# Optimization experiments

Hardware: AMD Instinct MI355X
Metric: run time of the kernel (lower is better)

The kernel has to match this reference:

```python
import jax, jax.numpy as jnp
import numpy as np

INP = 512
HIDDEN = 512
N_HEADS = 8          # called 'head_dim' in the torch code
D_HEAD = HIDDEN // N_HEADS  # 64
BASE = 10000.0
SCALE = D_HEAD ** (-0.5)


def rope(x):
    # x: [b, s, h, d]
    b, s, h, d = x.shape
    half = d // 2
    theta = 1.0 / (BASE ** (jnp.arange(0, d, 2, dtype=jnp.float32) / d))  # [d/2]
    idx_theta = jnp.arange(s, dtype=jnp.float32)[:, None] * theta[None, :]  # [s, d/2]
    idx_theta2 = jnp.concatenate([idx_theta, idx_theta], axis=1)            # [s, d]
    neg_half = jnp.concatenate([-x[..., half:], x[..., :half]], axis=-1)
    cos = jnp.cos(idx_theta2)[None, :, None, :]
    sin = jnp.sin(idx_theta2)[None, :, None, :]
    return x * cos + neg_half * sin


def setup_inputs() -> dict:
    key = jax.random.key(0)
    ks = jax.random.split(key, 10)
    b, s = 4, 2048
    init = lambda k, shp, fan_in: jax.random.normal(k, shp, jnp.float32) * (fan_in ** -0.5)
    return {
        "x": jax.random.normal(ks[0], (b, s, INP), jnp.float32),
        "c": jax.random.normal(ks[1], (b, s, INP), jnp.float32),
        "Wq": init(ks[2], (INP, HIDDEN), INP), "bq": jnp.zeros((HIDDEN,), jnp.float32),
        "Wk": init(ks[3], (INP, HIDDEN), INP), "bk": jnp.zeros((HIDDEN,), jnp.float32),
        "Wv": init(ks[4], (INP, HIDDEN), INP), "bv": jnp.zeros((HIDDEN,), jnp.float32),
        "Wo": init(ks[5], (HIDDEN, INP), HIDDEN), "bo": jnp.zeros((INP,), jnp.float32),
    }


def reference(x, c, Wq, bq, Wk, bk, Wv, bv, Wo, bo):
    b, s, _ = x.shape
    h_res = x
    q = (c @ Wq + bq).reshape(b, s, N_HEADS, D_HEAD)
    k = (x @ Wk + bk).reshape(b, s, N_HEADS, D_HEAD)
    v = (x @ Wv + bv).reshape(b, s, N_HEADS, D_HEAD)
    q = rope(q)
    k = rope(k)  # computed but unused, exactly as in the source
    # NOTE: source computes scores between q and V (not k) -- faithful reproduction
    att = jnp.einsum('bihd,bjhd->bhij', q, v)            # [b, h, s, s]
    att = jax.nn.softmax(att * SCALE, axis=-1)
    out = jnp.einsum('bhij,bjhd->bihd', att, v)          # [b, s, h, d]
    out = out.reshape(b, s, HIDDEN)
    out = out @ Wo + bo
    return out + h_res
```

## Files before the change

### kernel.cpp

```cpp
#include <hip/hip_runtime.h>
#include <hip/hip_bf16.h>
#include <cstdint>

typedef float f32x4 __attribute__((ext_vector_type(4)));
typedef float f32x16 __attribute__((ext_vector_type(16)));
typedef short bf16x8 __attribute__((ext_vector_type(8)));
typedef short bf16x4 __attribute__((ext_vector_type(4)));
typedef unsigned int u32x2 __attribute__((ext_vector_type(2)));
typedef unsigned short u16;

#define B_    4
#define S_    2048
#define H_    8
#define D_    64
#define M_    8192

#define OFF_CBF   0UL
#define OFF_XBF   8388608UL
#define OFF_QBH   16777216UL
#define OFF_VBH   25165824UL
#define OFF_VTBH  33554432UL
#define OFF_ATTN  41943040UL
#define OFF_WQT   50331648UL
#define OFF_WVT   50855936UL
#define OFF_WOT   51380224UL
#define OFF_BIAS  51904512UL
#define OFF_COS   51910656UL
#define OFF_SIN   52172800UL
#define WS_NEEDED 52434944UL

__device__ __forceinline__ u16 f2bf(float f){
    union { float f; uint32_t u; } v; v.f = f;
    uint32_t r = (v.u + 0x7fffu + ((v.u >> 16) & 1u)) >> 16;
    return (u16)r;
}
__device__ __forceinline__ float bf2f(u16 h){
    union { uint32_t u; float f; } v; v.u = ((uint32_t)h) << 16;
    return v.f;
}

__device__ __forceinline__ uint32_t cvtpk(float lo, float hi){
    uint32_t r;
    asm("v_cvt_pk_bf16_f32 %0, %1, %2" : "=v"(r) : "v"(lo), "v"(hi));
    return r;
}
__device__ __forceinline__ void plswap(uint32_t &va, uint32_t &vb){
#if __has_builtin(__builtin_amdgcn_permlane32_swap)
    u32x2 r = __builtin_amdgcn_permlane32_swap(va, vb, false, false);
    va = r[0]; vb = r[1];
#else
    asm volatile("v_permlane32_swap_b32 %0, %1" : "+v"(va), "+v"(vb));
#endif
}

__device__ __forceinline__ int swz(int row, int col){
    return (col & ~63) | ((((col >> 3) & 7) ^ (row & 7)) << 3) | (col & 7);
}

__device__ __forceinline__ int detect_f32(const void* x_in){
    int lane = threadIdx.x & 63;
    ushort2 dv = ((const ushort2*)x_in)[lane];
    bool hit = ((((dv.x >> 7) & 0xFF) >= 160) || (((dv.y >> 7) & 0xFF) >= 160));
    return __ballot(hit) != 0ULL;
}

__device__ __forceinline__ void gload_lds16(const u16* g, u16* l){
    __builtin_amdgcn_global_load_lds(
        (const __attribute__((address_space(1))) void*)g,
        (__attribute__((address_space(3))) void*)l, 16, 0, 0);
}

__global__ void k_prep(const void* c_in, const void* x_in,
                       const void* Wq, const void* Wv, const void* Wo,
                       const void* bq, const void* bv, const void* bo,
                       u16* c_bf, u16* x_bf,
                       u16* Wqt, u16* Wvt, u16* Wot, float* bias_ws,
                       float* cos_t, float* sin_t){
    int bid = blockIdx.x;
    if (bid >= 11264){
        int idx = (bid - 11264) * 256 + threadIdx.x;
        int pos = idx >> 5, j = idx & 31;
        double theta = pow(10000.0, -(double)j / 32.0);
        double rev = ((double)pos * theta) * 0.15915494309189535;
        rev -= floor(rev);
        float fr = (float)rev;
        cos_t[idx] = __builtin_amdgcn_cosf(fr);
        sin_t[idx] = __builtin_amdgcn_sinf(fr);
        return;
    }
    if (bid >= 8192){
        int f = detect_f32(x_in);
        int wi = (bid - 8192) >> 10;
        int idx = ((bid - 8192) & 1023) * 256 + threadIdx.x;
        int k = idx >> 9, n = idx & 511;
        const void* W; u16* Wt; const void* bb;
        if (wi == 0){ W = Wq; Wt = Wqt; bb = bq; }
        else if (wi == 1){ W = Wv; Wt = Wvt; bb = bv; }
        else { W = Wo; Wt = Wot; bb = bo; }
        float v = f ? ((const float*)W)[idx] : bf2f(((const u16*)W)[idx]);
        Wt[n * 512 + (wi == 2 ? k : swz(n, k))] = f2bf(v);
        if (idx < 512){
            float b = f ? ((const float*)bb)[idx] : bf2f(((const u16*)bb)[idx]);
            bias_ws[wi * 512 + idx] = b;
        }
        return;
    }
    int f = detect_f32(x_in);
    int isx = bid >= 4096;
    int t = (bid & 4095) * 256 + threadIdx.x;
    const void* src = isx ? x_in : c_in;
    u16* dst = isx ? x_bf : c_bf;
    int e0 = t * 4, row = e0 >> 9, col = e0 & 511;
    size_t didx = (size_t)row * 512 + swz(row, col);
    ushort4 o;
    if (f){
        float4 v = ((const float4*)src)[t];
        o.x = f2bf(v.x); o.y = f2bf(v.y); o.z = f2bf(v.z); o.w = f2bf(v.w);
    } else {
        o = ((const ushort4*)src)[t];
    }
    *(ushort4*)(dst + didx) = o;
}

__global__ __launch_bounds__(256) void k_gemm_qv(
    const u16* __restrict__ c_bf, const u16* __restrict__ x_bf,
    const u16* __restrict__ Wqt, const u16* __restrict__ Wvt,
    const float* __restrict__ bias_ws,
    const float* __restrict__ cos_t, const float* __restrict__ sin_t,
    u16* __restrict__ Qbh, u16* __restrict__ Vbh, u16* __restrict__ Vtbh)
{
    __shared__ __align__(16) u16 Als[2][128 * 64];
    __shared__ __align__(16) u16 Bls[2][128 * 64];
    const int w = threadIdx.x >> 6, lane = threadIdx.x & 63;
    const int g = lane >> 4, cq = lane & 15;
    const int wm = w & 1, wn = w >> 1;
    const int z = blockIdx.z;
    const u16* A  = z ? x_bf : c_bf;
    const u16* Wt = z ? Wvt : Wqt;
    const float* bias = bias_ws + (z ? 512 : 0);
    const int m0b = blockIdx.x * 128, n0b = blockIdx.y * 128;
    const int m0 = m0b + wm * 64, n0 = n0b + wn * 64;
    const int swzi = ((cq & 7) << 3);

    int srow[4], scol[4];
    #pragma unroll
    for (int i = 0; i < 4; i++){
        int flat = (w * 4 + i) * 64 + lane;
        srow[i] = flat >> 3; scol[i] = (flat & 7) * 8;
    }

    const f32x4 zero = {0.f, 0.f, 0.f, 0.f};
    f32x4 acc[4][4];
    #pragma unroll
    for (int i = 0; i < 4; i++)
        #pragma unroll
        for (int j = 0; j < 4; j++) acc[i][j] = zero;

    #pragma unroll
    for (int i = 0; i < 4; i++){
        gload_lds16(A  + (size_t)(m0b + srow[i]) * 512 + scol[i], &Als[0][(w*4 + i) * 512]);
        gload_lds16(Wt + (size_t)(n0b + srow[i]) * 512 + scol[i], &Bls[0][(w*4 + i) * 512]);
    }

    for (int kt = 0; kt < 8; kt++){
        const int buf = kt & 1;
        __builtin_amdgcn_s_waitcnt(0x0F70);
        __syncthreads();
        if (kt < 7){
            const int kk = (kt + 1) * 64;
            #pragma unroll
            for (int i = 0; i < 4; i++){
                gload_lds16(A  + (size_t)(m0b + srow[i]) * 512 + kk + scol[i], &Als[buf^1][(w*4 + i) * 512]);
                gload_lds16(Wt + (size_t)(n0b + srow[i]) * 512 + kk + scol[i], &Bls[buf^1][(w*4 + i) * 512]);
            }
        }
        #pragma unroll
        for (int ks = 0; ks < 2; ks++){
            const int cs = ((ks * 4 + g) << 3) ^ swzi;
            bf16x8 a[4], b[4];
            #pragma unroll
            for (int mt = 0; mt < 4; mt++)
                a[mt] = *(const bf16x8*)&Als[buf][(wm*64 + mt*16 + cq) * 64 + cs];
            #pragma unroll
            for (int nt = 0; nt < 4; nt++)
                b[nt] = *(const bf16x8*)&Bls[buf][(wn*64 + nt*16 + cq) * 64 + cs];
            #pragma unroll
            for (int mt = 0; mt < 4; mt++)
                #pragma unroll
                for (int nt = 0; nt < 4; nt++)
                    acc[mt][nt] = __builtin_amdgcn_mfma_f32_16x16x32_bf16(a[mt], b[nt], acc[mt][nt], 0, 0, 0);
        }
    }
    __syncthreads();

    #pragma unroll
    for (int nt = 0; nt < 4; nt++){
        float bvv = bias[n0 + nt*16 + cq];
        #pragma unroll
        for (int mt = 0; mt < 4; mt++) acc[mt][nt] += bvv;
    }
    const int h = n0 >> 6;
    if (z == 0){
        const float SCL = 0.125f * 1.4426950408889634f;
        #pragma unroll
        for (int mt = 0; mt < 4; mt++){
            #pragma unroll
            for (int r = 0; r < 4; r++){
                int row = m0 + mt*16 + g*4 + r;
                int b_idx = row >> 11, si = row & 2047;
                size_t base = ((size_t)(b_idx*8 + h) * 2048 + si) * 64;
                #pragma unroll
                for (int nt = 0; nt < 2; nt++){
                    int dj = nt*16 + cq;
                    float cv = cos_t[si*32 + dj], sv = sin_t[si*32 + dj];
                    float x1 = acc[mt][nt][r], x2 = acc[mt][nt+2][r];
                    Qbh[base + dj]      = f2bf((x1*cv - x2*sv) * SCL);
                    Qbh[base + dj + 32] = f2bf((x2*cv + x1*sv) * SCL);
                }
            }
        }
    } else {
        float* ltw = ((float*)&Als[0][0]) + w * (16 * 65);
        const int b_idx = m0 >> 11, si0 = m0 & 2047;
        const size_t tbase = ((size_t)(b_idx*8 + h) * 64) * 2048;
        #pragma unroll
        for (int mt = 0; mt < 4; mt++)
            #pragma unroll
            for (int r = 0; r < 4; r++){
                int row = m0 + mt*16 + g*4 + r;
                int bi = row >> 11, si = row & 2047;
                size_t base = ((size_t)(bi*8 + h) * 2048 + si) * 64;
                #pragma unroll
                for (int nt = 0; nt < 4; nt++)
                    Vbh[base + nt*16 + cq] = f2bf(acc[mt][nt][r]);
            }
        #pragma unroll
        for (int nt = 0; nt < 4; nt++){
            #pragma unroll
            for (int mt = 0; mt < 4; mt++)
                #pragma unroll
                for (int r = 0; r < 4; r++)
                    ltw[cq * 65 + mt*16 + g*4 + r] = acc[mt][nt][r];
            __builtin_amdgcn_wave_barrier();
            #pragma unroll
            for (int dd = 0; dd < 16; dd++){
                float v = ltw[dd * 65 + lane];
                Vtbh[tbase + (size_t)(nt*16 + dd) * 2048 + si0 + lane] = f2bf(v);
            }
            __builtin_amdgcn_wave_barrier();
        }
    }
}

__global__ __launch_bounds__(256, 2) void k_attn(
    const u16* __restrict__ Qbh, const u16* __restrict__ Vbh,
    const u16* __restrict__ Vtbh,
    u16* __restrict__ part0, u16* __restrict__ part1, float* __restrict__ lsum)
{
    __shared__ __align__(16) u16 Vs[2][64 * 68];
    __shared__ __align__(16) u16 Vts[2][64 * 68];

    const int bid = blockIdx.x;
    const int logical = (bid & 7) * 64 + (bid >> 3);
    const int xb = logical & 7;
    const int bh = (logical >> 3) & 31;
    const int z  = logical >> 8;

    const int w = threadIdx.x >> 6, lane = threadIdx.x & 63;
    const int r32 = lane & 31, hl = lane >> 5;
    const int i0 = xb * 256 + w * 64;
    const int j0 = z * 1024;

    bf16x8 aq[2][4];
    #pragma unroll
    for (int it = 0; it < 2; it++)
        #pragma unroll
        for (int kk = 0; kk < 4; kk++)
            aq[it][kk] = *(const bf16x8*)(Qbh + ((size_t)bh*2048 + i0 + it*32 + r32)*64 + kk*16 + hl*8);

    const int sr = w * 16 + (lane >> 2), sc = (lane & 3) * 16;
    const u16* gvs = Vbh  + ((size_t)bh*2048 + j0 + sr) * 64 + sc;
    const u16* gvt = Vtbh + ((size_t)bh*64 + sr) * 2048 + j0 + sc;
    const int ls = sr * 68 + sc;

    {
        bf16x8 a0 = *(const bf16x8*)gvs,       a1 = *(const bf16x8*)(gvs + 8);
        bf16x8 b0 = *(const bf16x8*)gvt,       b1 = *(const bf16x8*)(gvt + 8);
        *(bf16x8*)&Vs[0][ls]  = a0;  *(bf16x8*)&Vs[0][ls + 8]  = a1;
        *(bf16x8*)&Vts[0][ls] = b0;  *(bf16x8*)&Vts[0][ls + 8] = b1;
    }

    f32x16 ot[2][2];
    #pragma unroll
    for (int it = 0; it < 2; it++)
        #pragma unroll
        for (int dt = 0; dt < 2; dt++)
            #pragma unroll
            for (int rr = 0; rr < 16; rr++) ot[it][dt][rr] = 0.f;
    const f32x16 zero16 = ot[0][0];
    float fl[2] = {0.f, 0.f};

    for (int jt = 0; jt < 16; jt++){
        const int buf = jt & 1;
        __syncthreads();
        bf16x8 na0, na1, nb0, nb1;
        if (jt < 15){
            na0 = *(const bf16x8*)(gvs + (size_t)(jt + 1) * 4096);
            na1 = *(const bf16x8*)(gvs + (size_t)(jt + 1) * 4096 + 8);
            nb0 = *(const bf16x8*)(gvt + (size_t)(jt + 1) * 64);
            nb1 = *(const bf16x8*)(gvt + (size_t)(jt + 1) * 64 + 8);
        }
        bf16x8 pb[2][4];
        #pragma unroll
        for (int jtile = 0; jtile < 2; jtile++){
            bf16x8 vf[4];
            #pragma unroll
            for (int kk = 0; kk < 4; kk++)
                vf[kk] = *(const bf16x8*)&Vs[buf][(jtile*32 + r32)*68 + kk*16 + hl*8];
            f32x16 st0 = zero16, st1 = zero16;
            __builtin_amdgcn_s_setprio(1);
            #pragma unroll
            for (int kk = 0; kk < 4; kk++){
                st0 = __builtin_amdgcn_mfma_f32_32x32x16_bf16(vf[kk], aq[0][kk], st0, 0, 0, 0);
                st1 = __builtin_amdgcn_mfma_f32_32x32x16_bf16(vf[kk], aq[1][kk], st1, 0, 0, 0);
            }
            __builtin_amdgcn_s_setprio(0);
            #pragma unroll
            for (int rr = 0; rr < 16; rr++) st0[rr] = __builtin_amdgcn_exp2f(st0[rr]);
            #pragma unroll
            for (int rr = 0; rr < 16; rr++) st1[rr] = __builtin_amdgcn_exp2f(st1[rr]);
            {
                float a0 = (st0[0]+st0[1]) + (st0[2]+st0[3]);
                float a1 = (st0[4]+st0[5]) + (st0[6]+st0[7]);
                float a2 = (st0[8]+st0[9]) + (st0[10]+st0[11]);
                float a3 = (st0[12]+st0[13]) + (st0[14]+st0[15]);
                fl[0] += (a0+a1) + (a2+a3);
                float b0 = (st1[0]+st1[1]) + (st1[2]+st1[3]);
                float b1 = (st1[4]+st1[5]) + (st1[6]+st1[7]);
                float b2 = (st1[8]+st1[9]) + (st1[10]+st1[11]);
                float b3 = (st1[12]+st1[13]) + (st1[14]+st1[15]);
                fl[1] += (b0+b1) + (b2+b3);
            }
            #pragma unroll
            for (int c = 0; c < 2; c++){
                uint32_t dA1 = cvtpk(st0[c*8+0], st0[c*8+1]);
                uint32_t dA2 = cvtpk(st0[c*8+2], st0[c*8+3]);
                uint32_t dB1 = cvtpk(st0[c*8+4], st0[c*8+5]);
                uint32_t dB2 = cvtpk(st0[c*8+6], st0[c*8+7]);
                plswap(dA1, dB1);
                plswap(dA2, dB2);
                union { bf16x8 v; uint32_t d[4]; } u;
                u.d[0] = dA1; u.d[1] = dA2; u.d[2] = dB1; u.d[3] = dB2;
                pb[0][jtile*2 + c] = u.v;
            }
            #pragma unroll
            for (int c = 0; c < 2; c++){
                uint32_t dA1 = cvtpk(st1[c*8+0], st1[c*8+1]);
                uint32_t dA2 = cvtpk(st1[c*8+2], st1[c*8+3]);
                uint32_t dB1 = cvtpk(st1[c*8+4], st1[c*8+5]);
                uint32_t dB2 = cvtpk(st1[c*8+6], st1[c*8+7]);
                plswap(dA1, dB1);
                plswap(dA2, dB2);
                union { bf16x8 v; uint32_t d[4]; } u;
                u.d[0] = dA1; u.d[1] = dA2; u.d[2] = dB1; u.d[3] = dB2;
                pb[1][jtile*2 + c] = u.v;
            }
        }
        __builtin_amdgcn_s_setprio(1);
        #pragma unroll
        for (int c = 0; c < 4; c++){
            bf16x8 vt0 = *(const bf16x8*)&Vts[buf][r32*68 + c*16 + hl*8];
            bf16x8 vt1 = *(const bf16x8*)&Vts[buf][(32 + r32)*68 + c*16 + hl*8];
            ot[0][0] = __builtin_amdgcn_mfma_f32_32x32x16_bf16(vt0, pb[0][c], ot[0][0], 0, 0, 0);
            ot[1][0] = __builtin_amdgcn_mfma_f32_32x32x16_bf16(vt0, pb[1][c], ot[1][0], 0, 0, 0);
            ot[0][1] = __builtin_amdgcn_mfma_f32_32x32x16_bf16(vt1, pb[0][c], ot[0][1], 0, 0, 0);
            ot[1][1] = __builtin_amdgcn_mfma_f32_32x32x16_bf16(vt1, pb[1][c], ot[1][1], 0, 0, 0);
        }
        __builtin_amdgcn_s_setprio(0);
        if (jt < 15){
            *(bf16x8*)&Vs[buf^1][ls]  = na0;  *(bf16x8*)&Vs[buf^1][ls + 8]  = na1;
            *(bf16x8*)&Vts[buf^1][ls] = nb0;  *(bf16x8*)&Vts[buf^1][ls + 8] = nb1;
        }
    }
    const int b_idx = bh >> 3, hh = bh & 7;
    u16* part = z ? part1 : part0;
    #pragma unroll
    for (int it = 0; it < 2; it++){
        float sum = fl[it] + __shfl_xor(fl[it], 32);
        const int row = b_idx*2048 + i0 + it*32 + r32;
        if (lane < 32)
            lsum[(size_t)z*65536 + (size_t)hh*8192 + row] = sum;
        #pragma unroll
        for (int dt = 0; dt < 2; dt++){
            #pragma unroll
            for (int q = 0; q < 4; q++){
                float v0 = ot[it][dt][q*4+0];
                float v1 = ot[it][dt][q*4+1];
                float v2 = ot[it][dt][q*4+2];
                float v3 = ot[it][dt][q*4+3];
                uint2 pw;
                pw.x = cvtpk(v0, v1);
                pw.y = cvtpk(v2, v3);
                int col = hh*64 + dt*32 + q*8 + hl*4;
                *(uint2*)&part[(size_t)row * 512 + col] = pw;
            }
        }
    }
}

__global__ __launch_bounds__(256) void k_gemm_out(
    const u16* __restrict__ part0, const u16* __restrict__ part1,
    const float* __restrict__ lsum,
    const u16* __restrict__ Wot, const float* __restrict__ bias_ws,
    const void* __restrict__ x_in, void* __restrict__ out)
{
    __shared__ __align__(16) u16 Als[2][128 * 68];
    __shared__ __align__(16) u16 Bls[2][64 * 68];
    const int w = threadIdx.x >> 6, lane = threadIdx.x & 63;
    const int g = lane >> 4, cq = lane & 15;
    const int wm = w & 1, wn = w >> 1;
    const int m0b = blockIdx.x * 128, n0b = blockIdx.y * 64;
    const int m0 = m0b + wm * 64, n0 = n0b + wn * 32;
    const int f = detect_f32(x_in);

    int sra[4], sca[4], srb[2], scb[2];
    #pragma unroll
    for (int i = 0; i < 4; i++){
        int flat = (w * 4 + i) * 64 + lane;
        sra[i] = flat >> 3; sca[i] = (flat & 7) * 8;
    }
    #pragma unroll
    for (int i = 0; i < 2; i++){
        int flat = (w * 2 + i) * 64 + lane;
        srb[i] = flat >> 3; scb[i] = (flat & 7) * 8;
    }

    const f32x4 zero = {0.f, 0.f, 0.f, 0.f};
    f32x4 acc[4][2];
    #pragma unroll
    for (int i = 0; i < 4; i++)
        #pragma unroll
        for (int j = 0; j < 2; j++) acc[i][j] = zero;

    bf16x8 pa0[4], pa1[4], pb[2]; float pr[4];
    #pragma unroll
    for (int i = 0; i < 4; i++){
        int row = m0b + sra[i];
        pa0[i] = *(const bf16x8*)&part0[(size_t)row * 512 + sca[i]];
        pa1[i] = *(const bf16x8*)&part1[(size_t)row * 512 + sca[i]];
        pr[i] = 1.f / (lsum[row] + lsum[65536 + row]);
    }
    #pragma unroll
    for (int i = 0; i < 2; i++)
        pb[i] = *(const bf16x8*)&Wot[(size_t)(n0b + srb[i]) * 512 + scb[i]];
    #pragma unroll
    for (int i = 0; i < 4; i++){
        union { bf16x8 v; u16 e[8]; } a8;
        #pragma unroll
        for (int e = 0; e < 8; e++)
            a8.e[e] = f2bf((bf2f((u16)pa0[i][e]) + bf2f((u16)pa1[i][e])) * pr[i]);
        *(bf16x8*)&Als[0][sra[i]*68 + sca[i]] = a8.v;
    }
    #pragma unroll
    for (int i = 0; i < 2; i++)
        *(bf16x8*)&Bls[0][srb[i]*68 + scb[i]] = pb[i];

    for (int kt = 0; kt < 8; kt++){
        const int buf = kt & 1;
        __syncthreads();
        if (kt < 7){
            const int kk = (kt + 1) * 64, h = kt + 1;
            #pragma unroll
            for (int i = 0; i < 4; i++){
                int row = m0b + sra[i];
                pa0[i] = *(const bf16x8*)&part0[(size_t)row * 512 + kk + sca[i]];
                pa1[i] = *(const bf16x8*)&part1[(size_t)row * 512 + kk + sca[i]];
                pr[i] = 1.f / (lsum[(size_t)h*8192 + row] + lsum[65536 + (size_t)h*8192 + row]);
            }
            #pragma unroll
            for (int i = 0; i < 2; i++)
                pb[i] = *(const bf16x8*)&Wot[(size_t)(n0b + srb[i]) * 512 + kk + scb[i]];
        }
        #pragma unroll
        for (int ks = 0; ks < 2; ks++){
            bf16x8 a[4], b[2];
            #pragma unroll
            for (int mt = 0; mt < 4; mt++)
                a[mt] = *(const bf16x8*)&Als[buf][(wm*64 + mt*16 + cq)*68 + ks*32 + g*8];
            #pragma unroll
            for (int nt = 0; nt < 2; nt++)
                b[nt] = *(const bf16x8*)&Bls[buf][(wn*32 + nt*16 + cq)*68 + ks*32 + g*8];
            #pragma unroll
            for (int mt = 0; mt < 4; mt++)
                #pragma unroll
                for (int nt = 0; nt < 2; nt++)
                    acc[mt][nt] = __builtin_amdgcn_mfma_f32_16x16x32_bf16(a[mt], b[nt], acc[mt][nt], 0, 0, 0);
        }
        if (kt < 7){
            #pragma unroll
            for (int i = 0; i < 4; i++){
                union { bf16x8 v; u16 e[8]; } a8;
                #pragma unroll
                for (int e = 0; e < 8; e++)
                    a8.e[e] = f2bf((bf2f((u16)pa0[i][e]) + bf2f((u16)pa1[i][e])) * pr[i]);
                *(bf16x8*)&Als[buf^1][sra[i]*68 + sca[i]] = a8.v;
            }
            #pragma unroll
            for (int i = 0; i < 2; i++)
                *(bf16x8*)&Bls[buf^1][srb[i]*68 + scb[i]] = pb[i];
        }
    }
    #pragma unroll
    for (int mt = 0; mt < 4; mt++)
        #pragma unroll
        for (int nt = 0; nt < 2; nt++)
            #pragma unroll
            for (int r = 0; r < 4; r++){
                int row = m0 + mt*16 + g*4 + r;
                int col = n0 + nt*16 + cq;
                size_t idx = (size_t)row * 512 + col;
                float resid = f ? ((const float*)x_in)[idx] : bf2f(((const u16*)x_in)[idx]);
                float v = acc[mt][nt][r] + bias_ws[1024 + col] + resid;
                if (f) ((float*)out)[idx] = v;
                else   ((u16*)out)[idx] = f2bf(v);
            }
}

extern "C" void kernel_launch(void* const* d_in, const int* in_sizes, int n_in,
                              void* d_out, int out_size, void* d_ws, size_t ws_size,
                              hipStream_t stream){
    const void* x_in = d_in[0];
    const void* c_in = d_in[1];
    const void* Wq = d_in[2]; const void* bq = d_in[3];
    const void* Wv = d_in[6]; const void* bv = d_in[7];
    const void* Wo = d_in[8]; const void* bo = d_in[9];

    if (ws_size < WS_NEEDED){
        hipMemsetAsync(d_out, 0, (size_t)out_size * 2, stream);
        return;
    }
    char* ws = (char*)d_ws;
    u16* c_bf  = (u16*)(ws + OFF_CBF);
    u16* x_bf  = (u16*)(ws + OFF_XBF);
    u16* Qbh   = (u16*)(ws + OFF_QBH);
    u16* Vbh   = (u16*)(ws + OFF_VBH);
    u16* Vtbh  = (u16*)(ws + OFF_VTBH);
    u16* part0 = (u16*)(ws + OFF_ATTN);
    u16* part1 = (u16*)(ws + OFF_CBF);
    float* lsum = (float*)(ws + OFF_XBF);
    u16* Wqt   = (u16*)(ws + OFF_WQT);
    u16* Wvt   = (u16*)(ws + OFF_WVT);
    u16* Wot   = (u16*)(ws + OFF_WOT);
    float* bias_ws = (float*)(ws + OFF_BIAS);
    float* cos_t   = (float*)(ws + OFF_COS);
    float* sin_t   = (float*)(ws + OFF_SIN);

    k_prep<<<11520, 256, 0, stream>>>(c_in, x_in, Wq, Wv, Wo, bq, bv, bo,
                                      c_bf, x_bf, Wqt, Wvt, Wot, bias_ws, cos_t, sin_t);
    k_gemm_qv<<<dim3(64, 4, 2), 256, 0, stream>>>(c_bf, x_bf, Wqt, Wvt, bias_ws,
                                                  cos_t, sin_t, Qbh, Vbh, Vtbh);
    k_attn<<<dim3(512), 256, 0, stream>>>(Qbh, Vbh, Vtbh, part0, part1, lsum);
    k_gemm_out<<<dim3(64, 8), 256, 0, stream>>>(part0, part1, lsum, Wot, bias_ws,
                                                x_in, d_out);
}
```

Before: 182.0 us.

## Software-pipeline attention loop so PV MFMAs of previous tile overlap next QV and exp

Restructures the attention main loop into a prologue, steady state, and epilogue. Each iteration now runs the P·V MFMAs for the previous tile, using the previous buffer, interleaved with the score MFMAs for the current tile, so matrix work overlaps the exp2 and packing work. The Q projection epilogue also stores Q in an interleaved packed layout with one cvt_pk per pair, and the attention kernel de-interleaves it on load. In exchange it adds an extra __syncthreads per iteration and raises register pressure because pb is live across iterations.

```diff
diff --git a/kernel.cpp b/kernel.cpp
--- a/kernel.cpp
+++ b/kernel.cpp
@@ -51,6 +51,24 @@
 #else
     asm volatile("v_permlane32_swap_b32 %0, %1" : "+v"(va), "+v"(vb));
 #endif
+}
+
+__device__ __forceinline__ f32x16 mfma32(bf16x8 a, bf16x8 b, f32x16 c){
+    return __builtin_amdgcn_mfma_f32_32x32x16_bf16(a, b, c, 0, 0, 0);
+}
+
+__device__ __forceinline__ void deint(uint4 a, uint4 b, bf16x8 &lo, bf16x8 &hi){
+    union { bf16x8 v; uint32_t d[4]; } L, H;
+    uint32_t s0=a.x, s1=a.y, s2=a.z, s3=a.w, s4=b.x, s5=b.y, s6=b.z, s7=b.w;
+    L.d[0] = (s0 & 0xffffu) | (s1 << 16);
+    L.d[1] = (s2 & 0xffffu) | (s3 << 16);
+    L.d[2] = (s4 & 0xffffu) | (s5 << 16);
+    L.d[3] = (s6 & 0xffffu) | (s7 << 16);
+    H.d[0] = (s0 >> 16) | (s1 & 0xffff0000u);
+    H.d[1] = (s2 >> 16) | (s3 & 0xffff0000u);
+    H.d[2] = (s4 >> 16) | (s5 & 0xffff0000u);
+    H.d[3] = (s6 >> 16) | (s7 & 0xffff0000u);
+    lo = L.v; hi = H.v;
 }
 
 __device__ __forceinline__ int swz(int row, int col){
@@ -202,20 +220,20 @@
     const int h = n0 >> 6;
     if (z == 0){
         const float SCL = 0.125f * 1.4426950408889634f;
+        uint32_t* Qpk = (uint32_t*)Qbh;
         #pragma unroll
         for (int mt = 0; mt < 4; mt++){
             #pragma unroll
             for (int r = 0; r < 4; r++){
                 int row = m0 + mt*16 + g*4 + r;
                 int b_idx = row >> 11, si = row & 2047;
-                size_t base = ((size_t)(b_idx*8 + h) * 2048 + si) * 64;
+                size_t base = ((size_t)(b_idx*8 + h) * 2048 + si) * 32;
                 #pragma unroll
                 for (int nt = 0; nt < 2; nt++){
                     int dj = nt*16 + cq;
                     float cv = cos_t[si*32 + dj], sv = sin_t[si*32 + dj];
                     float x1 = acc[mt][nt][r], x2 = acc[mt][nt+2][r];
-                    Qbh[base + dj]      = f2bf((x1*cv - x2*sv) * SCL);
-                    Qbh[base + dj + 32] = f2bf((x2*cv + x1*sv) * SCL);
+                    Qpk[base + dj] = cvtpk((x1*cv - x2*sv) * SCL, (x2*cv + x1*sv) * SCL);
                 }
             }
         }
@@ -271,12 +289,18 @@
     const int i0 = xb * 256 + w * 64;
     const int j0 = z * 1024;
 
+    const uint32_t* Qpk = (const uint32_t*)Qbh;
     bf16x8 aq[2][4];
     #pragma unroll
-    for (int it = 0; it < 2; it++)
-        #pragma unroll
-        for (int kk = 0; kk < 4; kk++)
-            aq[it][kk] = *(const bf16x8*)(Qbh + ((size_t)bh*2048 + i0 + it*32 + r32)*64 + kk*16 + hl*8);
+    for (int it = 0; it < 2; it++){
+        size_t qb = ((size_t)bh*2048 + i0 + it*32 + r32)*32 + hl*8;
+        uint4 a0 = *(const uint4*)&Qpk[qb];
+        uint4 a1 = *(const uint4*)&Qpk[qb + 4];
+        uint4 b0 = *(const uint4*)&Qpk[qb + 16];
+        uint4 b1 = *(const uint4*)&Qpk[qb + 20];
+        deint(a0, a1, aq[it][0], aq[it][2]);
+        deint(b0, b1, aq[it][1], aq[it][3]);
+    }
 
     const int sr = w * 16 + (lane >> 2), sc = (lane & 3) * 16;
     const u16* gvs = Vbh  + ((size_t)bh*2048 + j0 + sr) * 64 + sc;
@@ -299,9 +323,65 @@
             for (int rr = 0; rr < 16; rr++) ot[it][dt][rr] = 0.f;
     const f32x16 zero16 = ot[0][0];
     float fl[2] = {0.f, 0.f};
-
-    for (int jt = 0; jt < 16; jt++){
-        const int buf = jt & 1;
+    bf16x8 pb[2][4];
+
+    {
+        bf16x8 na0 = *(const bf16x8*)(gvs + 4096);
+        bf16x8 na1 = *(const bf16x8*)(gvs + 4096 + 8);
+        bf16x8 nb0 = *(const bf16x8*)(gvt + 64);
+        bf16x8 nb1 = *(const bf16x8*)(gvt + 64 + 8);
+        __syncthreads();
+        #pragma unroll
+        for (int jtile = 0; jtile < 2; jtile++){
+            bf16x8 vf[4];
+            #pragma unroll
+            for (int kk = 0; kk < 4; kk++)
+                vf[kk] = *(const bf16x8*)&Vs[0][(jtile*32 + r32)*68 + kk*16 + hl*8];
+            f32x16 st0 = zero16, st1 = zero16;
+            __builtin_amdgcn_s_setprio(1);
+            #pragma unroll
+            for (int kk = 0; kk < 4; kk++){
+                st0 = mfma32(vf[kk], aq[0][kk], st0);
+                st1 = mfma32(vf[kk], aq[1][kk], st1);
+            }
+            __builtin_amdgcn_s_setprio(0);
+            #pragma unroll
+            for (int rr = 0; rr < 16; rr++) st0[rr] = __builtin_amdgcn_exp2f(st0[rr]);
+            #pragma unroll
+            for (int rr = 0; rr < 16; rr++) st1[rr] = __builtin_amdgcn_exp2f(st1[rr]);
+            fl[0] += ((st0[0]+st0[1])+(st0[2]+st0[3])) + ((st0[4]+st0[5])+(st0[6]+st0[7]))
+                   + ((st0[8]+st0[9])+(st0[10]+st0[11])) + ((st0[12]+st0[13])+(st0[14]+st0[15]));
+            fl[1] += ((st1[0]+st1[1])+(st1[2]+st1[3])) + ((st1[4]+st1[5])+(st1[6]+st1[7]))
+                   + ((st1[8]+st1[9])+(st1[10]+st1[11])) + ((st1[12]+st1[13])+(st1[14]+st1[15]));
+            #pragma unroll
+            for (int c = 0; c < 2; c++){
+                uint32_t dA1 = cvtpk(st0[c*8+0], st0[c*8+1]);
+                uint32_t dA2 = cvtpk(st0[c*8+2], st0[c*8+3]);
+                uint32_t dB1 = cvtpk(st0[c*8+4], st0[c*8+5]);
+                uint32_t dB2 = cvtpk(st0[c*8+6], st0[c*8+7]);
+                plswap(dA1, dB1); plswap(dA2, dB2);
+                union { bf16x8 v; uint32_t d[4]; } u;
+                u.d[0] = dA1; u.d[1] = dA2; u.d[2] = dB1; u.d[3] = dB2;
+                pb[0][jtile*2 + c] = u.v;
+            }
+            #pragma unroll
+            for (int c = 0; c < 2; c++){
+                uint32_t dA1 = cvtpk(st1[c*8+0], st1[c*8+1]);
+                uint32_t dA2 = cvtpk(st1[c*8+2], st1[c*8+3]);
+                uint32_t dB1 = cvtpk(st1[c*8+4], st1[c*8+5]);
+                uint32_t dB2 = cvtpk(st1[c*8+6], st1[c*8+7]);
+                plswap(dA1, dB1); plswap(dA2, dB2);
+                union { bf16x8 v; uint32_t d[4]; } u;
+                u.d[0] = dA1; u.d[1] = dA2; u.d[2] = dB1; u.d[3] = dB2;
+                pb[1][jtile*2 + c] = u.v;
+            }
+        }
+        *(bf16x8*)&Vs[1][ls]  = na0;  *(bf16x8*)&Vs[1][ls + 8]  = na1;
+        *(bf16x8*)&Vts[1][ls] = nb0;  *(bf16x8*)&Vts[1][ls + 8] = nb1;
+    }
+
+    for (int jt = 1; jt < 16; jt++){
+        const int bufA = jt & 1, bufB = bufA ^ 1;
         __syncthreads();
         bf16x8 na0, na1, nb0, nb1;
         if (jt < 15){
@@ -310,45 +390,45 @@
             nb0 = *(const bf16x8*)(gvt + (size_t)(jt + 1) * 64);
             nb1 = *(const bf16x8*)(gvt + (size_t)(jt + 1) * 64 + 8);
         }
-        bf16x8 pb[2][4];
         #pragma unroll
         for (int jtile = 0; jtile < 2; jtile++){
             bf16x8 vf[4];
             #pragma unroll
             for (int kk = 0; kk < 4; kk++)
-                vf[kk] = *(const bf16x8*)&Vs[buf][(jtile*32 + r32)*68 + kk*16 + hl*8];
+                vf[kk] = *(const bf16x8*)&Vs[bufA][(jtile*32 + r32)*68 + kk*16 + hl*8];
             f32x16 st0 = zero16, st1 = zero16;
             __builtin_amdgcn_s_setprio(1);
             #pragma unroll
             for (int kk = 0; kk < 4; kk++){
-                st0 = __builtin_amdgcn_mfma_f32_32x32x16_bf16(vf[kk], aq[0][kk], st0, 0, 0, 0);
-                st1 = __builtin_amdgcn_mfma_f32_32x32x16_bf16(vf[kk], aq[1][kk], st1, 0, 0, 0);
+                st0 = mfma32(vf[kk], aq[0][kk], st0);
+                st1 = mfma32(vf[kk], aq[1][kk], st1);
+            }
+            #pragma unroll
+            for (int cc = 0; cc < 2; cc++){
+                const int c = jtile*2 + cc;
+                bf16x8 vt0 = *(const bf16x8*)&Vts[bufB][r32*68 + c*16 + hl*8];
+                bf16x8 vt1 = *(const bf16x8*)&Vts[bufB][(32 + r32)*68 + c*16 + hl*8];
+                ot[0][0] = mfma32(vt0, pb[0][c], ot[0][0]);
+                ot[1][0] = mfma32(vt0, pb[1][c], ot[1][0]);
+                ot[0][1] = mfma32(vt1, pb[0][c], ot[0][1]);
+                ot[1][1] = mfma32(vt1, pb[1][c], ot[1][1]);
             }
             __builtin_amdgcn_s_setprio(0);
             #pragma unroll
             for (int rr = 0; rr < 16; rr++) st0[rr] = __builtin_amdgcn_exp2f(st0[rr]);
             #pragma unroll
             for (int rr = 0; rr < 16; rr++) st1[rr] = __builtin_amdgcn_exp2f(st1[rr]);
-            {
-                float a0 = (st0[0]+st0[1]) + (st0[2]+st0[3]);
-                float a1 = (st0[4]+st0[5]) + (st0[6]+st0[7]);
-                float a2 = (st0[8]+st0[9]) + (st0[10]+st0[11]);
-                float a3 = (st0[12]+st0[13]) + (st0[14]+st0[15]);
-                fl[0] += (a0+a1) + (a2+a3);
-                float b0 = (st1[0]+st1[1]) + (st1[2]+st1[3]);
-                float b1 = (st1[4]+st1[5]) + (st1[6]+st1[7]);
-                float b2 = (st1[8]+st1[9]) + (st1[10]+st1[11]);
-                float b3 = (st1[12]+st1[13]) + (st1[14]+st1[15]);
-                fl[1] += (b0+b1) + (b2+b3);
-            }
+            fl[0] += ((st0[0]+st0[1])+(st0[2]+st0[3])) + ((st0[4]+st0[5])+(st0[6]+st0[7]))
+                   + ((st0[8]+st0[9])+(st0[10]+st0[11])) + ((st0[12]+st0[13])+(st0[14]+st0[15]));
+            fl[1] += ((st1[0]+st1[1])+(st1[2]+st1[3])) + ((st1[4]+st1[5])+(st1[6]+st1[7]))
+                   + ((st1[8]+st1[9])+(st1[10]+st1[11])) + ((st1[12]+st1[13])+(st1[14]+st1[15]));
             #pragma unroll
             for (int c = 0; c < 2; c++){
                 uint32_t dA1 = cvtpk(st0[c*8+0], st0[c*8+1]);
                 uint32_t dA2 = cvtpk(st0[c*8+2], st0[c*8+3]);
                 uint32_t dB1 = cvtpk(st0[c*8+4], st0[c*8+5]);
                 uint32_t dB2 = cvtpk(st0[c*8+6], st0[c*8+7]);
-                plswap(dA1, dB1);
-                plswap(dA2, dB2);
+                plswap(dA1, dB1); plswap(dA2, dB2);
                 union { bf16x8 v; uint32_t d[4]; } u;
                 u.d[0] = dA1; u.d[1] = dA2; u.d[2] = dB1; u.d[3] = dB2;
                 pb[0][jtile*2 + c] = u.v;
@@ -359,29 +439,31 @@
                 uint32_t dA2 = cvtpk(st1[c*8+2], st1[c*8+3]);
                 uint32_t dB1 = cvtpk(st1[c*8+4], st1[c*8+5]);
                 uint32_t dB2 = cvtpk(st1[c*8+6], st1[c*8+7]);
-                plswap(dA1, dB1);
-                plswap(dA2, dB2);
+                plswap(dA1, dB1); plswap(dA2, dB2);
                 union { bf16x8 v; uint32_t d[4]; } u;
                 u.d[0] = dA1; u.d[1] = dA2; u.d[2] = dB1; u.d[3] = dB2;
                 pb[1][jtile*2 + c] = u.v;
             }
         }
-        __builtin_amdgcn_s_setprio(1);
-        #pragma unroll
-        for (int c = 0; c < 4; c++){
-            bf16x8 vt0 = *(const bf16x8*)&Vts[buf][r32*68 + c*16 + hl*8];
-            bf16x8 vt1 = *(const bf16x8*)&Vts[buf][(32 + r32)*68 + c*16 + hl*8];
-            ot[0][0] = __builtin_amdgcn_mfma_f32_32x32x16_bf16(vt0, pb[0][c], ot[0][0], 0, 0, 0);
-            ot[1][0] = __builtin_amdgcn_mfma_f32_32x32x16_bf16(vt0, pb[1][c], ot[1][0], 0, 0, 0);
-            ot[0][1] = __builtin_amdgcn_mfma_f32_32x32x16_bf16(vt1, pb[0][c], ot[0][1], 0, 0, 0);
-            ot[1][1] = __builtin_amdgcn_mfma_f32_32x32x16_bf16(vt1, pb[1][c], ot[1][1], 0, 0, 0);
-        }
-        __builtin_amdgcn_s_setprio(0);
+        __syncthreads();
         if (jt < 15){
-            *(bf16x8*)&Vs[buf^1][ls]  = na0;  *(bf16x8*)&Vs[buf^1][ls + 8]  = na1;
-            *(bf16x8*)&Vts[buf^1][ls] = nb0;  *(bf16x8*)&Vts[buf^1][ls + 8] = nb1;
-        }
-    }
+            *(bf16x8*)&Vs[bufB][ls]  = na0;  *(bf16x8*)&Vs[bufB][ls + 8]  = na1;
+            *(bf16x8*)&Vts[bufB][ls] = nb0;  *(bf16x8*)&Vts[bufB][ls + 8] = nb1;
+        }
+    }
+
+    __builtin_amdgcn_s_setprio(1);
+    #pragma unroll
+    for (int c = 0; c < 4; c++){
+        bf16x8 vt0 = *(const bf16x8*)&Vts[1][r32*68 + c*16 + hl*8];
+        bf16x8 vt1 = *(const bf16x8*)&Vts[1][(32 + r32)*68 + c*16 + hl*8];
+        ot[0][0] = mfma32(vt0, pb[0][c], ot[0][0]);
+        ot[1][0] = mfma32(vt0, pb[1][c], ot[1][0]);
+        ot[0][1] = mfma32(vt1, pb[0][c], ot[0][1]);
+        ot[1][1] = mfma32(vt1, pb[1][c], ot[1][1]);
+    }
+    __builtin_amdgcn_s_setprio(0);
+
     const int b_idx = bh >> 3, hh = bh & 7;
     u16* part = z ? part1 : part0;
     #pragma unroll
```

Measured after the change: 181.1 us, median of 2. Within noise of the previous version (-0.5%).
